# Kernel optimization log

Hardware: AMD Instinct MI355X
Metric: run time of the kernel (lower is better)

Reference implementation:

```python
import jax, jax.numpy as jnp
import numpy as np

# Mamba block hyperparams (canonical: expand=2, d_state=16, d_conv=4, dt_rank=d_model/16)
D_MODEL = 1024
D_INNER = 2 * D_MODEL          # 2048
D_STATE = 16
D_CONV = 4
DT_RANK = D_MODEL // 16        # 64
B, L = 2, 1024


def setup_inputs() -> dict:
    key = jax.random.key(0)
    ks = jax.random.split(key, 12)
    s = lambda fan_in: 1.0 / np.sqrt(fan_in)
    x = jax.random.normal(ks[0], (B, L, D_MODEL), dtype=jnp.float32)
    W_in = jax.random.normal(ks[1], (D_MODEL, 2 * D_INNER), dtype=jnp.float32) * s(D_MODEL)
    conv_w = jax.random.normal(ks[2], (D_INNER, 1, D_CONV), dtype=jnp.float32) * s(D_CONV)
    conv_b = jax.random.normal(ks[3], (D_INNER,), dtype=jnp.float32) * 0.02
    W_xp = jax.random.normal(ks[4], (D_INNER, DT_RANK + 2 * D_STATE), dtype=jnp.float32) * s(D_INNER)
    W_dt = jax.random.normal(ks[5], (DT_RANK, D_INNER), dtype=jnp.float32) * s(DT_RANK)
    # dt bias init so softplus(dt_bias) ~ uniform in [1e-3, 1e-1] (mamba convention)
    dt = jnp.exp(jax.random.uniform(ks[6], (D_INNER,)) * (np.log(0.1) - np.log(1e-3)) + np.log(1e-3))
    dt_bias = dt + jnp.log(-jnp.expm1(-dt))  # inverse softplus
    A_log = jnp.log(jnp.broadcast_to(jnp.arange(1, D_STATE + 1, dtype=jnp.float32), (D_INNER, D_STATE)))
    D_skip = jnp.ones((D_INNER,), dtype=jnp.float32)
    W_out = jax.random.normal(ks[7], (D_INNER, D_MODEL), dtype=jnp.float32) * s(D_INNER)
    return {"x": x, "W_in": W_in, "conv_w": conv_w, "conv_b": conv_b, "W_xp": W_xp,
            "W_dt": W_dt, "dt_bias": dt_bias, "A_log": A_log, "D_skip": D_skip, "W_out": W_out}


def _causal_depthwise_conv(u, conv_w, conv_b):
    # u: [B, E, L], conv_w: [E, 1, K] depthwise, causal (left-pad K-1)
    K = conv_w.shape[-1]
    u = jnp.pad(u, ((0, 0), (0, 0), (K - 1, 0)))
    y = jax.lax.conv_general_dilated(
        u, conv_w, window_strides=(1,), padding='VALID',
        dimension_numbers=('NCH', 'OIH', 'NCH'), feature_group_count=u.shape[1])
    return y + conv_b[None, :, None]


def _selective_scan(u, delta, A, Bm, Cm, D_skip):
    # u, delta: [B,L,E]; A: [E,N]; Bm, Cm: [B,L,N]; D_skip: [E]
    dA = jnp.exp(jnp.einsum('ble,en->blen', delta, A))          # [B,L,E,N]
    dBu = jnp.einsum('ble,bln,ble->blen', delta, Bm, u)          # [B,L,E,N]

    def step(h, inp):
        dA_t, dBu_t, C_t = inp                                    # [B,E,N],[B,E,N],[B,N]
        h = dA_t * h + dBu_t
        y_t = jnp.einsum('ben,bn->be', h, C_t)
        return h, y_t

    h0 = jnp.zeros((u.shape[0], A.shape[0], A.shape[1]), dtype=u.dtype)
    xs = (jnp.swapaxes(dA, 0, 1), jnp.swapaxes(dBu, 0, 1), jnp.swapaxes(Cm, 0, 1))
    _, ys = jax.lax.scan(step, h0, xs)                            # ys: [L,B,E]
    y = jnp.swapaxes(ys, 0, 1)                                    # [B,L,E]
    return y + u * D_skip[None, None, :]


def reference(x, W_in, conv_w, conv_b, W_xp, W_dt, dt_bias, A_log, D_skip, W_out):
    # in_proj and gate split
    xz = x @ W_in                                                 # [B,L,2E]
    xp, z = jnp.split(xz, 2, axis=-1)                             # [B,L,E] each
    # causal depthwise conv + silu
    u = _causal_depthwise_conv(jnp.swapaxes(xp, 1, 2), conv_w, conv_b)
    u = jax.nn.silu(jnp.swapaxes(u, 1, 2))                        # [B,L,E]
    # input-dependent dt, B, C
    x_dbl = u @ W_xp                                              # [B,L,R+2N]
    dt_r, Bm, Cm = jnp.split(x_dbl, [DT_RANK, DT_RANK + D_STATE], axis=-1)
    delta = jax.nn.softplus(dt_r @ W_dt + dt_bias)                # [B,L,E]
    A = -jnp.exp(A_log)                                           # [E,N]
    y = _selective_scan(u, delta, A, Bm, Cm, D_skip)              # [B,L,E]
    # gate and out_proj
    y = y * jax.nn.silu(z)
    return y @ W_out                                              # [B,L,D]
```

## Files before the change

### kernel.cpp

```cpp
#include <hip/hip_runtime.h>
#include <math.h>

#define D_MODEL 1024
#define D_INNER 2048
#define D_STATE 16
#define D_CONV  4
#define DT_RANK 64
#define BB      2
#define LL      1024
#define BL      (BB*LL)
#define CHUNK   16
#define NCHUNK  (LL/CHUNK)
#define KSPLIT  16

typedef __attribute__((ext_vector_type(8))) short short8;
typedef __attribute__((ext_vector_type(4))) float f32x4;
typedef unsigned short ushort_t;
typedef unsigned int uint_t;

__device__ __forceinline__ float sigmoidf_(float x) { return 1.0f / (1.0f + __expf(-x)); }

__device__ __forceinline__ ushort_t f2bf(float f) {
    uint_t u = __float_as_uint(f);
    uint_t r = (u + 0x7fffu + ((u >> 16) & 1u)) >> 16;
    return (ushort_t)r;
}

__device__ __forceinline__ void gload_lds16(const void* g, void* l) {
    __builtin_amdgcn_global_load_lds(
        (const __attribute__((address_space(1))) void*)g,
        (__attribute__((address_space(3))) void*)l,
        16, 0, 0);
}

template<int BM, int BN, int SPLIT>
__global__ __launch_bounds__(256)
void gemm_bf16_t(const ushort_t* __restrict__ A, const ushort_t* __restrict__ Bt,
                 float* __restrict__ C0, float* __restrict__ C1,
                 int M, int N, int K, int split) {
    constexpr int WMr = BM / 32;
    constexpr int WNr = BN / 32;
    const int nx = N / BN;
    const int nwg = nx * (M / BM);
    const int wg = ((blockIdx.x & 7) * (nwg >> 3)) + (blockIdx.x >> 3);
    const int row0 = (wg / nx) * BM;
    const int col0 = (wg % nx) * BN;

    __shared__ __align__(16) ushort_t As[BM * 32];
    __shared__ __align__(16) ushort_t Bs[BN * 32];

    const int tid  = threadIdx.x;
    const int lane = tid & 63;
    const int wave = tid >> 6;
    const int wr = wave >> 1, wc = wave & 1;

    f32x4 acc[WMr][WNr];
    #pragma unroll
    for (int m = 0; m < WMr; ++m)
        #pragma unroll
        for (int n = 0; n < WNr; ++n)
            acc[m][n] = (f32x4){0.f, 0.f, 0.f, 0.f};

    const ushort_t* Ablk = A  + (size_t)row0 * K;
    const ushort_t* Bblk = Bt + (size_t)col0 * K;
    const int r_ld  = tid >> 2;
    const int c8_ld = (tid & 3) * 8;

    for (int k0 = 0; k0 < K; k0 += 32) {
        #pragma unroll
        for (int i = 0; i < BM / 64; ++i)
            gload_lds16(Ablk + (size_t)(i * 64 + r_ld) * K + k0 + c8_ld,
                        &As[(i * 64 + wave * 16) * 32]);
        #pragma unroll
        for (int i = 0; i < BN / 64; ++i)
            gload_lds16(Bblk + (size_t)(i * 64 + r_ld) * K + k0 + c8_ld,
                        &Bs[(i * 64 + wave * 16) * 32]);
        __syncthreads();

        short8 af[WMr], bf[WNr];
        const int fr = lane & 15;
        const int kb = (lane >> 4) * 8;
        #pragma unroll
        for (int m = 0; m < WMr; ++m)
            af[m] = *(const short8*)&As[(wr * WMr * 16 + m * 16 + fr) * 32 + kb];
        #pragma unroll
        for (int n = 0; n < WNr; ++n)
            bf[n] = *(const short8*)&Bs[(wc * WNr * 16 + n * 16 + fr) * 32 + kb];

        #pragma unroll
        for (int m = 0; m < WMr; ++m)
            #pragma unroll
            for (int n = 0; n < WNr; ++n)
                acc[m][n] = __builtin_amdgcn_mfma_f32_16x16x32_bf16(
                    af[m], bf[n], acc[m][n], 0, 0, 0);
        __syncthreads();
    }

    float* Cb; int ldc, cb;
    if (SPLIT && col0 >= split) { Cb = C1; ldc = N - split; cb = col0 - split; }
    else if (SPLIT)             { Cb = C0; ldc = split;     cb = col0; }
    else                        { Cb = C0; ldc = N;         cb = col0; }

    const int crow = (lane >> 4) * 4;
    const int ccol = lane & 15;
    #pragma unroll
    for (int m = 0; m < WMr; ++m) {
        #pragma unroll
        for (int n = 0; n < WNr; ++n) {
            float* cp = Cb + (size_t)(row0 + wr * WMr * 16 + m * 16 + crow) * ldc
                           + cb + wc * WNr * 16 + n * 16 + ccol;
            #pragma unroll
            for (int i = 0; i < 4; ++i)
                cp[(size_t)i * ldc] = acc[m][n][i];
        }
    }
}

__global__ __launch_bounds__(256)
void f32_to_bf16(const float* __restrict__ in, ushort_t* __restrict__ out, int n) {
    int i = (blockIdx.x * 256 + threadIdx.x) * 8;
    if (i + 8 <= n) {
        float4 a = *reinterpret_cast<const float4*>(in + i);
        float4 b = *reinterpret_cast<const float4*>(in + i + 4);
        ushort_t o[8] = {f2bf(a.x), f2bf(a.y), f2bf(a.z), f2bf(a.w),
                         f2bf(b.x), f2bf(b.y), f2bf(b.z), f2bf(b.w)};
        *reinterpret_cast<short8*>(out + i) = *reinterpret_cast<short8*>(o);
    }
}

__global__ __launch_bounds__(256)
void transp_bf16(const float* __restrict__ W, ushort_t* __restrict__ Wt,
                 int R, int C) {
    __shared__ ushort_t tile[32][33];
    int tx = threadIdx.x & 31, ty = threadIdx.x >> 5;
    int r0 = blockIdx.y * 32, c0 = blockIdx.x * 32;
    #pragma unroll
    for (int i = 0; i < 32; i += 8)
        tile[ty + i][tx] = f2bf(W[(size_t)(r0 + ty + i) * C + c0 + tx]);
    __syncthreads();
    #pragma unroll
    for (int i = 0; i < 32; i += 8)
        Wt[(size_t)(c0 + ty + i) * R + r0 + tx] = tile[tx][ty + i];
}

__global__ __launch_bounds__(256)
void gemm_xdbl_splitk(const float* __restrict__ u, const float* __restrict__ W,
                      float* __restrict__ part) {
    __shared__ float As[16][65];
    __shared__ float Bs[16][96];

    const int tid = threadIdx.x;
    const int m0 = blockIdx.x * 64;
    const int kbase = blockIdx.y * (D_INNER / KSPLIT);

    const int tx = tid & 15;
    const int ty = tid >> 4;
    const int arow = tid >> 4;
    const int acol = tid & 15;

    float acc[4][6] = {};

    for (int k0 = 0; k0 < D_INNER / KSPLIT; k0 += 16) {
        #pragma unroll
        for (int p = 0; p < 4; ++p) {
            int r = arow + p * 16;
            As[acol][r] = u[(size_t)(m0 + r) * D_INNER + kbase + k0 + acol];
        }
        #pragma unroll
        for (int j = 0; j < 6; ++j) {
            int idx = j * 256 + tid;
            int row = idx / 96, col = idx - row * 96;
            Bs[row][col] = W[(size_t)(kbase + k0 + row) * 96 + col];
        }
        __syncthreads();
        #pragma unroll
        for (int kk = 0; kk < 16; ++kk) {
            float a[4], b[6];
            #pragma unroll
            for (int i = 0; i < 4; ++i) a[i] = As[kk][ty * 4 + i];
            #pragma unroll
            for (int j = 0; j < 6; ++j) b[j] = Bs[kk][tx * 6 + j];
            #pragma unroll
            for (int i = 0; i < 4; ++i)
                #pragma unroll
                for (int j = 0; j < 6; ++j)
                    acc[i][j] = fmaf(a[i], b[j], acc[i][j]);
        }
        __syncthreads();
    }

    float* pblk = part + (size_t)blockIdx.y * BL * 96;
    #pragma unroll
    for (int i = 0; i < 4; ++i)
        #pragma unroll
        for (int j = 0; j < 6; ++j)
            pblk[(size_t)(m0 + ty * 4 + i) * 96 + tx * 6 + j] = acc[i][j];
}

__global__ __launch_bounds__(256)
void xdbl_reduce(const float* __restrict__ part, float* __restrict__ x_dbl) {
    int i = blockIdx.x * 256 + threadIdx.x;
    float s = 0.0f;
    #pragma unroll
    for (int k = 0; k < KSPLIT; ++k)
        s += part[(size_t)k * BL * 96 + i];
    x_dbl[i] = s;
}

template<int EPI>
__global__ __launch_bounds__(256)
void gemm_f32(const float* __restrict__ A, const float* __restrict__ B,
              float* __restrict__ C, const float* __restrict__ bias,
              int M, int N, int K, int lda, int ldb, int ldc) {
    __shared__ float As[16][65];
    __shared__ float Bs[16][64];

    const int tid = threadIdx.x;
    const int tx = tid & 15;
    const int ty = tid >> 4;
    const int row0 = blockIdx.y * 64;
    const int col0 = blockIdx.x * 64;

    const int arow = tid >> 4;
    const int acol = tid & 15;
    const int brow = tid >> 6;
    const int bcol = tid & 63;

    float acc[4][4] = {};

    for (int k0 = 0; k0 < K; k0 += 16) {
        #pragma unroll
        for (int p = 0; p < 4; ++p) {
            int r = arow + p * 16;
            As[acol][r] = A[(size_t)(row0 + r) * lda + (k0 + acol)];
        }
        int gc = col0 + bcol;
        #pragma unroll
        for (int p = 0; p < 4; ++p) {
            int r = brow + p * 4;
            Bs[r][bcol] = (gc < N) ? B[(size_t)(k0 + r) * ldb + gc] : 0.0f;
        }
        __syncthreads();
        #pragma unroll
        for (int kk = 0; kk < 16; ++kk) {
            float a[4];
            #pragma unroll
            for (int i = 0; i < 4; ++i) a[i] = As[kk][ty * 4 + i];
            float4 bv = *reinterpret_cast<const float4*>(&Bs[kk][tx * 4]);
            float b4[4] = {bv.x, bv.y, bv.z, bv.w};
            #pragma unroll
            for (int i = 0; i < 4; ++i)
                #pragma unroll
                for (int j = 0; j < 4; ++j)
                    acc[i][j] = fmaf(a[i], b4[j], acc[i][j]);
        }
        __syncthreads();
    }

    #pragma unroll
    for (int i = 0; i < 4; ++i) {
        int gr = row0 + ty * 4 + i;
        #pragma unroll
        for (int j = 0; j < 4; ++j) {
            int gc = col0 + tx * 4 + j;
            if (gc < N) {
                float v = acc[i][j];
                if (EPI == 1) {
                    v += bias[gc];
                    v = (v > 20.0f) ? v : log1pf(__expf(v));
                }
                C[(size_t)gr * ldc + gc] = v;
            }
        }
    }
}

__global__ __launch_bounds__(256)
void conv_silu(const float* __restrict__ xp, const float* __restrict__ conv_w,
               const float* __restrict__ conv_b, float* __restrict__ u) {
    int idx = blockIdx.x * 256 + threadIdx.x;
    if (idx >= BL * D_INNER) return;
    int e  = idx & (D_INNER - 1);
    int bl = idx >> 11;
    int b = bl >> 10, l = bl & (LL - 1);
    float acc = conv_b[e];
    #pragma unroll
    for (int k = 0; k < D_CONV; ++k) {
        int ll = l - (D_CONV - 1) + k;
        if (ll >= 0)
            acc = fmaf(conv_w[e * D_CONV + k],
                       xp[(size_t)(b * LL + ll) * D_INNER + e], acc);
    }
    u[idx] = acc * sigmoidf_(acc);
}

__global__ __launch_bounds__(256)
void scan_phase1(const float* __restrict__ delta, const float* __restrict__ u_in,
                 const float* __restrict__ x_dbl, const float* __restrict__ A_log,
                 float* __restrict__ hend, float* __restrict__ sumdelta) {
    int g = blockIdx.x * 256 + threadIdx.x;
    int e = g & (D_INNER - 1);
    int c = (g >> 11) & (NCHUNK - 1);
    int b = g >> 17;

    float A_en[D_STATE];
    #pragma unroll
    for (int n = 0; n < D_STATE; n += 4) {
        float4 al = *(const float4*)&A_log[e * D_STATE + n];
        A_en[n]     = -__expf(al.x);
        A_en[n + 1] = -__expf(al.y);
        A_en[n + 2] = -__expf(al.z);
        A_en[n + 3] = -__expf(al.w);
    }

    float h[D_STATE];
    #pragma unroll
    for (int n = 0; n < D_STATE; ++n) h[n] = 0.0f;
    float S = 0.0f;

    const int t0 = c * CHUNK;
    const float* dptr = delta + (size_t)(b * LL + t0) * D_INNER + e;
    const float* uptr = u_in  + (size_t)(b * LL + t0) * D_INNER + e;
    const float* xb   = x_dbl + (size_t)(b * LL + t0) * 96 + DT_RANK;

    for (int t = 0; t < CHUNK; ++t) {
        float dv = dptr[(size_t)t * D_INNER];
        float uv = uptr[(size_t)t * D_INNER];
        const float* xrow = xb + (size_t)t * 96;
        float4 B0 = *(const float4*)(xrow);
        float4 B1 = *(const float4*)(xrow + 4);
        float4 B2 = *(const float4*)(xrow + 8);
        float4 B3 = *(const float4*)(xrow + 12);
        float Bv[16] = {B0.x, B0.y, B0.z, B0.w, B1.x, B1.y, B1.z, B1.w,
                        B2.x, B2.y, B2.z, B2.w, B3.x, B3.y, B3.z, B3.w};
        S += dv;
        float du = dv * uv;
        #pragma unroll
        for (int n = 0; n < D_STATE; ++n) {
            float dA = __expf(dv * A_en[n]);
            h[n] = fmaf(dA, h[n], du * Bv[n]);
        }
    }

    size_t rbase = ((size_t)(c * BB + b) * D_STATE) * D_INNER + e;
    #pragma unroll
    for (int n = 0; n < D_STATE; ++n)
        hend[rbase + (size_t)n * D_INNER] = h[n];
    sumdelta[(size_t)(c * BB + b) * D_INNER + e] = S;
}

__global__ __launch_bounds__(256)
void scan_phase2(const float* __restrict__ A_log, const float* __restrict__ sumdelta,
                 float* __restrict__ hh) {
    int g = blockIdx.x * 256 + threadIdx.x;
    int e = g & (D_INNER - 1);
    int n = (g >> 11) & (D_STATE - 1);
    int b = g >> 15;
    float A_en = -__expf(A_log[e * D_STATE + n]);
    float h = 0.0f;
    for (int c = 0; c < NCHUNK; ++c) {
        size_t idx = ((size_t)(c * BB + b) * D_STATE + n) * D_INNER + e;
        float he = hh[idx];
        float dA = __expf(A_en * sumdelta[(size_t)(c * BB + b) * D_INNER + e]);
        hh[idx] = h;
        h = fmaf(dA, h, he);
    }
}

__global__ __launch_bounds__(256)
void scan_phase3(const float* __restrict__ delta, const float* __restrict__ u_in,
                 const float* __restrict__ x_dbl, const float* __restrict__ z,
                 const float* __restrict__ A_log, const float* __restrict__ D_skip,
                 const float* __restrict__ hin, ushort_t* __restrict__ ybf) {
    int g = blockIdx.x * 256 + threadIdx.x;
    int e = g & (D_INNER - 1);
    int c = (g >> 11) & (NCHUNK - 1);
    int b = g >> 17;

    float A_en[D_STATE];
    #pragma unroll
    for (int n = 0; n < D_STATE; n += 4) {
        float4 al = *(const float4*)&A_log[e * D_STATE + n];
        A_en[n]     = -__expf(al.x);
        A_en[n + 1] = -__expf(al.y);
        A_en[n + 2] = -__expf(al.z);
        A_en[n + 3] = -__expf(al.w);
    }
    float D_e = D_skip[e];

    float h[D_STATE];
    size_t rbase = ((size_t)(c * BB + b) * D_STATE) * D_INNER + e;
    #pragma unroll
    for (int n = 0; n < D_STATE; ++n)
        h[n] = hin[rbase + (size_t)n * D_INNER];

    const int t0 = c * CHUNK;
    const float* dptr = delta + (size_t)(b * LL + t0) * D_INNER + e;
    const float* uptr = u_in  + (size_t)(b * LL + t0) * D_INNER + e;
    const float* xb   = x_dbl + (size_t)(b * LL + t0) * 96 + DT_RANK;
    const float* zptr = z     + (size_t)(b * LL + t0) * D_INNER + e;
    ushort_t* yout = ybf + (size_t)(b * LL + t0) * D_INNER + e;

    for (int t = 0; t < CHUNK; ++t) {
        float dv = dptr[(size_t)t * D_INNER];
        float uv = uptr[(size_t)t * D_INNER];
        const float* xrow = xb + (size_t)t * 96;
        float4 B0 = *(const float4*)(xrow);
        float4 B1 = *(const float4*)(xrow + 4);
        float4 B2 = *(const float4*)(xrow + 8);
        float4 B3 = *(const float4*)(xrow + 12);
        float4 C0 = *(const float4*)(xrow + 16);
        float4 C1 = *(const float4*)(xrow + 20);
        float4 C2 = *(const float4*)(xrow + 24);
        float4 C3 = *(const float4*)(xrow + 28);
        float Bv[16] = {B0.x, B0.y, B0.z, B0.w, B1.x, B1.y, B1.z, B1.w,
                        B2.x, B2.y, B2.z, B2.w, B3.x, B3.y, B3.z, B3.w};
        float Cv[16] = {C0.x, C0.y, C0.z, C0.w, C1.x, C1.y, C1.z, C1.w,
                        C2.x, C2.y, C2.z, C2.w, C3.x, C3.y, C3.z, C3.w};
        float du = dv * uv;
        float y = 0.0f;
        #pragma unroll
        for (int n = 0; n < D_STATE; ++n) {
            float dA = __expf(dv * A_en[n]);
            h[n] = fmaf(dA, h[n], du * Bv[n]);
            y = fmaf(h[n], Cv[n], y);
        }
        float zv = zptr[(size_t)t * D_INNER];
        float yg = (y + uv * D_e) * (zv * sigmoidf_(zv));
        yout[(size_t)t * D_INNER] = f2bf(yg);
    }
}

extern "C" void kernel_launch(void* const* d_in, const int* in_sizes, int n_in,
                              void* d_out, int out_size, void* d_ws, size_t ws_size,
                              hipStream_t stream) {
    const float* x      = (const float*)d_in[0];
    const float* W_in   = (const float*)d_in[1];
    const float* conv_w = (const float*)d_in[2];
    const float* conv_b = (const float*)d_in[3];
    const float* W_xp   = (const float*)d_in[4];
    const float* W_dt   = (const float*)d_in[5];
    const float* dt_b   = (const float*)d_in[6];
    const float* A_log  = (const float*)d_in[7];
    const float* D_skip = (const float*)d_in[8];
    const float* W_out  = (const float*)d_in[9];
    float* out = (float*)d_out;

    const size_t M1 = 1024 * 1024;
    float* ws    = (float*)d_ws;
    float* z     = ws;
    float* hend  = ws + 4 * M1;
    float* xp    = hend;
    float* u     = ws + 8 * M1;
    float* x_dbl = ws + 12 * M1;
    float* sumd  = x_dbl + (size_t)BL * 96;
    ushort_t* ybf = (ushort_t*)(sumd + BB * NCHUNK * D_INNER);
    float* delta = ws + (14 * M1 + 512 * 1024);

    ushort_t* Wint_bf   = (ushort_t*)delta;
    ushort_t* x_bf      = (ushort_t*)(delta + 2 * M1);
    float*    xdbl_part = delta;
    ushort_t* Woutt_bf  = (ushort_t*)hend;

    dim3 blk(256);

    hipLaunchKernelGGL(f32_to_bf16, dim3((BL * D_MODEL) / (256 * 8)), blk, 0, stream,
                       x, x_bf, BL * D_MODEL);
    hipLaunchKernelGGL(transp_bf16, dim3(4096 / 32, 1024 / 32), blk, 0, stream,
                       W_in, Wint_bf, 1024, 4096);
    hipLaunchKernelGGL((gemm_bf16_t<64, 128, 1>),
                       dim3((BL / 64) * (4096 / 128)), blk, 0, stream,
                       x_bf, Wint_bf, xp, z, BL, 2 * D_INNER, D_MODEL, D_INNER);
    hipLaunchKernelGGL(conv_silu, dim3((BL * D_INNER) / 256), blk, 0, stream,
                       xp, conv_w, conv_b, u);
    hipLaunchKernelGGL(gemm_xdbl_splitk, dim3(BL / 64, KSPLIT), blk, 0, stream,
                       u, W_xp, xdbl_part);
    hipLaunchKernelGGL(xdbl_reduce, dim3((BL * 96) / 256), blk, 0, stream,
                       xdbl_part, x_dbl);
    hipLaunchKernelGGL((gemm_f32<1>), dim3(D_INNER / 64, BL / 64), blk, 0, stream,
                       x_dbl, W_dt, delta, dt_b, BL, D_INNER, DT_RANK, 96, D_INNER, D_INNER);
    hipLaunchKernelGGL(scan_phase1, dim3((BB * NCHUNK * D_INNER) / 256), blk, 0, stream,
                       delta, u, x_dbl, A_log, hend, sumd);
    hipLaunchKernelGGL(scan_phase2, dim3((BB * D_STATE * D_INNER) / 256), blk, 0, stream,
                       A_log, sumd, hend);
    hipLaunchKernelGGL(scan_phase3, dim3((BB * NCHUNK * D_INNER) / 256), blk, 0, stream,
                       delta, u, x_dbl, z, A_log, D_skip, hend, ybf);
    hipLaunchKernelGGL(transp_bf16, dim3(1024 / 32, 2048 / 32), blk, 0, stream,
                       W_out, Woutt_bf, 2048, 1024);
    hipLaunchKernelGGL((gemm_bf16_t<64, 64, 0>),
                       dim3((BL / 64) * (D_MODEL / 64)), blk, 0, stream,
                       ybf, Woutt_bf, out, out, BL, D_MODEL, D_INNER, D_MODEL);
}
```

Before: 197.0 us.

## Fuse conv+SiLU into consumers, store z in bf16, use geometric decay when A=-(n+1)

Removes the standalone conv_silu kernel and its u buffer. The conv and SiLU are now recomputed inside the x_dbl GEMM, with a 3-row halo staged in LDS, and inside both scan phases via a sliding window over xp. The in-projection GEMM writes the gate z as bf16, which halves that buffer's traffic but loses precision in the gate. The scan phases test at runtime whether A equals -(n+1) and, if so, replace 16 exps per step with one exp and repeated multiplies, which relies on the canonical A_log init.

Result: faster. 185.1 us (-6.0%).

```diff
diff --git a/kernel.cpp b/kernel.cpp
--- a/kernel.cpp
+++ b/kernel.cpp
@@ -12,6 +12,7 @@
 #define CHUNK   16
 #define NCHUNK  (LL/CHUNK)
 #define KSPLIT  16
+#define KS_E    (D_INNER/KSPLIT)
 
 typedef __attribute__((ext_vector_type(8))) short short8;
 typedef __attribute__((ext_vector_type(4))) float f32x4;
@@ -24,6 +25,9 @@
     uint_t u = __float_as_uint(f);
     uint_t r = (u + 0x7fffu + ((u >> 16) & 1u)) >> 16;
     return (ushort_t)r;
+}
+__device__ __forceinline__ float bf2f(ushort_t v) {
+    return __uint_as_float((uint_t)v << 16);
 }
 
 __device__ __forceinline__ void gload_lds16(const void* g, void* l) {
@@ -33,10 +37,10 @@
         16, 0, 0);
 }
 
-template<int BM, int BN, int SPLIT>
+template<int BM, int BN, int SPLIT, int BF0, int BF1>
 __global__ __launch_bounds__(256)
 void gemm_bf16_t(const ushort_t* __restrict__ A, const ushort_t* __restrict__ Bt,
-                 float* __restrict__ C0, float* __restrict__ C1,
+                 void* __restrict__ C0v, void* __restrict__ C1v,
                  int M, int N, int K, int split) {
     constexpr int WMr = BM / 32;
     constexpr int WNr = BN / 32;
@@ -96,22 +100,35 @@
         __syncthreads();
     }
 
-    float* Cb; int ldc, cb;
-    if (SPLIT && col0 >= split) { Cb = C1; ldc = N - split; cb = col0 - split; }
-    else if (SPLIT)             { Cb = C0; ldc = split;     cb = col0; }
-    else                        { Cb = C0; ldc = N;         cb = col0; }
-
     const int crow = (lane >> 4) * 4;
     const int ccol = lane & 15;
+    const bool second = SPLIT && (col0 >= split);
+    const int ldc = second ? (N - split) : (SPLIT ? split : N);
+    const int cb  = second ? (col0 - split) : col0;
+
     #pragma unroll
     for (int m = 0; m < WMr; ++m) {
         #pragma unroll
         for (int n = 0; n < WNr; ++n) {
-            float* cp = Cb + (size_t)(row0 + wr * WMr * 16 + m * 16 + crow) * ldc
-                           + cb + wc * WNr * 16 + n * 16 + ccol;
-            #pragma unroll
-            for (int i = 0; i < 4; ++i)
-                cp[(size_t)i * ldc] = acc[m][n][i];
+            size_t base = (size_t)(row0 + wr * WMr * 16 + m * 16 + crow) * ldc
+                          + cb + wc * WNr * 16 + n * 16 + ccol;
+            if (second) {
+                if (BF1) { ushort_t* cp = (ushort_t*)C1v + base;
+                    #pragma unroll
+                    for (int i = 0; i < 4; ++i) cp[(size_t)i * ldc] = f2bf(acc[m][n][i]);
+                } else { float* cp = (float*)C1v + base;
+                    #pragma unroll
+                    for (int i = 0; i < 4; ++i) cp[(size_t)i * ldc] = acc[m][n][i];
+                }
+            } else {
+                if (BF0) { ushort_t* cp = (ushort_t*)C0v + base;
+                    #pragma unroll
+                    for (int i = 0; i < 4; ++i) cp[(size_t)i * ldc] = f2bf(acc[m][n][i]);
+                } else { float* cp = (float*)C0v + base;
+                    #pragma unroll
+                    for (int i = 0; i < 4; ++i) cp[(size_t)i * ldc] = acc[m][n][i];
+                }
+            }
         }
     }
 }
@@ -144,27 +161,29 @@
 }
 
 __global__ __launch_bounds__(256)
-void gemm_xdbl_splitk(const float* __restrict__ u, const float* __restrict__ W,
-                      float* __restrict__ part) {
-    __shared__ float As[16][65];
+void gemm_xdbl_convfused(const float* __restrict__ xp, const float* __restrict__ W,
+                         const float* __restrict__ conv_w, const float* __restrict__ conv_b,
+                         float* __restrict__ part) {
+    __shared__ float Ax[16][68];
+    __shared__ float Au[16][65];
     __shared__ float Bs[16][96];
 
     const int tid = threadIdx.x;
     const int m0 = blockIdx.x * 64;
-    const int kbase = blockIdx.y * (D_INNER / KSPLIT);
-
+    const int kbase = blockIdx.y * KS_E;
     const int tx = tid & 15;
     const int ty = tid >> 4;
-    const int arow = tid >> 4;
-    const int acol = tid & 15;
+    const bool bhead = (m0 & (LL - 1)) == 0;
 
     float acc[4][6] = {};
 
-    for (int k0 = 0; k0 < D_INNER / KSPLIT; k0 += 16) {
-        #pragma unroll
-        for (int p = 0; p < 4; ++p) {
-            int r = arow + p * 16;
-            As[acol][r] = u[(size_t)(m0 + r) * D_INNER + kbase + k0 + acol];
+    for (int k0 = 0; k0 < KS_E; k0 += 16) {
+        for (int i = tid; i < 67 * 16; i += 256) {
+            int r = i >> 4, k = i & 15;
+            float v = 0.f;
+            if (!(bhead && r < 3))
+                v = xp[(size_t)(m0 - 3 + r) * D_INNER + kbase + k0 + k];
+            Ax[k][r] = v;
         }
         #pragma unroll
         for (int j = 0; j < 6; ++j) {
@@ -173,11 +192,26 @@
             Bs[row][col] = W[(size_t)(kbase + k0 + row) * 96 + col];
         }
         __syncthreads();
+        {
+            float4 w4 = *(const float4*)&conv_w[(size_t)(kbase + k0 + tx) * 4];
+            float cbv = conv_b[kbase + k0 + tx];
+            #pragma unroll
+            for (int rr = 0; rr < 4; ++rr) {
+                int r = ty + rr * 16;
+                float a = cbv;
+                a = fmaf(w4.x, Ax[tx][r], a);
+                a = fmaf(w4.y, Ax[tx][r + 1], a);
+                a = fmaf(w4.z, Ax[tx][r + 2], a);
+                a = fmaf(w4.w, Ax[tx][r + 3], a);
+                Au[tx][r] = a * sigmoidf_(a);
+            }
+        }
+        __syncthreads();
         #pragma unroll
         for (int kk = 0; kk < 16; ++kk) {
             float a[4], b[6];
             #pragma unroll
-            for (int i = 0; i < 4; ++i) a[i] = As[kk][ty * 4 + i];
+            for (int i = 0; i < 4; ++i) a[i] = Au[kk][ty * 4 + i];
             #pragma unroll
             for (int j = 0; j < 6; ++j) b[j] = Bs[kk][tx * 6 + j];
             #pragma unroll
@@ -276,26 +310,8 @@
 }
 
 __global__ __launch_bounds__(256)
-void conv_silu(const float* __restrict__ xp, const float* __restrict__ conv_w,
-               const float* __restrict__ conv_b, float* __restrict__ u) {
-    int idx = blockIdx.x * 256 + threadIdx.x;
-    if (idx >= BL * D_INNER) return;
-    int e  = idx & (D_INNER - 1);
-    int bl = idx >> 11;
-    int b = bl >> 10, l = bl & (LL - 1);
-    float acc = conv_b[e];
-    #pragma unroll
-    for (int k = 0; k < D_CONV; ++k) {
-        int ll = l - (D_CONV - 1) + k;
-        if (ll >= 0)
-            acc = fmaf(conv_w[e * D_CONV + k],
-                       xp[(size_t)(b * LL + ll) * D_INNER + e], acc);
-    }
-    u[idx] = acc * sigmoidf_(acc);
-}
-
-__global__ __launch_bounds__(256)
-void scan_phase1(const float* __restrict__ delta, const float* __restrict__ u_in,
+void scan_phase1(const float* __restrict__ delta, const float* __restrict__ xp,
+                 const float* __restrict__ conv_w, const float* __restrict__ conv_b,
                  const float* __restrict__ x_dbl, const float* __restrict__ A_log,
                  float* __restrict__ hend, float* __restrict__ sumdelta) {
     int g = blockIdx.x * 256 + threadIdx.x;
@@ -304,6 +320,7 @@
     int b = g >> 17;
 
     float A_en[D_STATE];
+    bool geo = true;
     #pragma unroll
     for (int n = 0; n < D_STATE; n += 4) {
         float4 al = *(const float4*)&A_log[e * D_STATE + n];
@@ -312,33 +329,78 @@
         A_en[n + 2] = -__expf(al.z);
         A_en[n + 3] = -__expf(al.w);
     }
+    #pragma unroll
+    for (int n = 0; n < D_STATE; ++n)
+        geo = geo && (fabsf(A_en[n] + (float)(n + 1)) <= 2e-5f * (float)(n + 1));
+
+    const int t0 = c * CHUNK;
+    const float* dptr = delta + (size_t)(b * LL + t0) * D_INNER + e;
+    const float* xptr = xp    + (size_t)(b * LL + t0) * D_INNER + e;
+    const float* xb   = x_dbl + (size_t)(b * LL + t0) * 96 + DT_RANK;
+    float4 w4 = *(const float4*)&conv_w[(size_t)e * 4];
+    float cbv = conv_b[e];
+
+    float xw0 = 0.f, xw1 = 0.f, xw2 = 0.f;
+    if (c > 0) {
+        xw0 = xptr[-3 * D_INNER];
+        xw1 = xptr[-2 * D_INNER];
+        xw2 = xptr[-1 * D_INNER];
+    }
 
     float h[D_STATE];
     #pragma unroll
     for (int n = 0; n < D_STATE; ++n) h[n] = 0.0f;
     float S = 0.0f;
 
-    const int t0 = c * CHUNK;
-    const float* dptr = delta + (size_t)(b * LL + t0) * D_INNER + e;
-    const float* uptr = u_in  + (size_t)(b * LL + t0) * D_INNER + e;
-    const float* xb   = x_dbl + (size_t)(b * LL + t0) * 96 + DT_RANK;
-
-    for (int t = 0; t < CHUNK; ++t) {
-        float dv = dptr[(size_t)t * D_INNER];
-        float uv = uptr[(size_t)t * D_INNER];
-        const float* xrow = xb + (size_t)t * 96;
-        float4 B0 = *(const float4*)(xrow);
-        float4 B1 = *(const float4*)(xrow + 4);
-        float4 B2 = *(const float4*)(xrow + 8);
-        float4 B3 = *(const float4*)(xrow + 12);
-        float Bv[16] = {B0.x, B0.y, B0.z, B0.w, B1.x, B1.y, B1.z, B1.w,
-                        B2.x, B2.y, B2.z, B2.w, B3.x, B3.y, B3.z, B3.w};
-        S += dv;
-        float du = dv * uv;
-        #pragma unroll
-        for (int n = 0; n < D_STATE; ++n) {
-            float dA = __expf(dv * A_en[n]);
-            h[n] = fmaf(dA, h[n], du * Bv[n]);
+    if (geo) {
+        for (int t = 0; t < CHUNK; ++t) {
+            float dv = dptr[(size_t)t * D_INNER];
+            float x0 = xptr[(size_t)t * D_INNER];
+            float a = cbv;
+            a = fmaf(w4.x, xw0, a); a = fmaf(w4.y, xw1, a);
+            a = fmaf(w4.z, xw2, a); a = fmaf(w4.w, x0, a);
+            float uv = a * sigmoidf_(a);
+            xw0 = xw1; xw1 = xw2; xw2 = x0;
+            const float* xrow = xb + (size_t)t * 96;
+            float4 B0 = *(const float4*)(xrow);
+            float4 B1 = *(const float4*)(xrow + 4);
+            float4 B2 = *(const float4*)(xrow + 8);
+            float4 B3 = *(const float4*)(xrow + 12);
+            float Bv[16] = {B0.x, B0.y, B0.z, B0.w, B1.x, B1.y, B1.z, B1.w,
+                            B2.x, B2.y, B2.z, B2.w, B3.x, B3.y, B3.z, B3.w};
+            S += dv;
+            float du = dv * uv;
+            float q = __expf(-dv);
+            float dA = q;
+            #pragma unroll
+            for (int n = 0; n < D_STATE; ++n) {
+                h[n] = fmaf(dA, h[n], du * Bv[n]);
+                dA *= q;
+            }
+        }
+    } else {
+        for (int t = 0; t < CHUNK; ++t) {
+            float dv = dptr[(size_t)t * D_INNER];
+            float x0 = xptr[(size_t)t * D_INNER];
+            float a = cbv;
+            a = fmaf(w4.x, xw0, a); a = fmaf(w4.y, xw1, a);
+            a = fmaf(w4.z, xw2, a); a = fmaf(w4.w, x0, a);
+            float uv = a * sigmoidf_(a);
+            xw0 = xw1; xw1 = xw2; xw2 = x0;
+            const float* xrow = xb + (size_t)t * 96;
+            float4 B0 = *(const float4*)(xrow);
+            float4 B1 = *(const float4*)(xrow + 4);
+            float4 B2 = *(const float4*)(xrow + 8);
+            float4 B3 = *(const float4*)(xrow + 12);
+            float Bv[16] = {B0.x, B0.y, B0.z, B0.w, B1.x, B1.y, B1.z, B1.w,
+                            B2.x, B2.y, B2.z, B2.w, B3.x, B3.y, B3.z, B3.w};
+            S += dv;
+            float du = dv * uv;
+            #pragma unroll
+            for (int n = 0; n < D_STATE; ++n) {
+                float dA = __expf(dv * A_en[n]);
+                h[n] = fmaf(dA, h[n], du * Bv[n]);
+            }
         }
     }
 
@@ -357,6 +419,8 @@
     int n = (g >> 11) & (D_STATE - 1);
     int b = g >> 15;
     float A_en = -__expf(A_log[e * D_STATE + n]);
+    float np1 = (float)(n + 1);
+    if (fabsf(A_en + np1) <= 2e-5f * np1) A_en = -np1;
     float h = 0.0f;
     for (int c = 0; c < NCHUNK; ++c) {
         size_t idx = ((size_t)(c * BB + b) * D_STATE + n) * D_INNER + e;
@@ -368,8 +432,9 @@
 }
 
 __global__ __launch_bounds__(256)
-void scan_phase3(const float* __restrict__ delta, const float* __restrict__ u_in,
-                 const float* __restrict__ x_dbl, const float* __restrict__ z,
+void scan_phase3(const float* __restrict__ delta, const float* __restrict__ xp,
+                 const float* __restrict__ conv_w, const float* __restrict__ conv_b,
+                 const float* __restrict__ x_dbl, const ushort_t* __restrict__ zbf,
                  const float* __restrict__ A_log, const float* __restrict__ D_skip,
                  const float* __restrict__ hin, ushort_t* __restrict__ ybf) {
     int g = blockIdx.x * 256 + threadIdx.x;
@@ -378,6 +443,7 @@
     int b = g >> 17;
 
     float A_en[D_STATE];
+    bool geo = true;
     #pragma unroll
     for (int n = 0; n < D_STATE; n += 4) {
         float4 al = *(const float4*)&A_log[e * D_STATE + n];
@@ -386,8 +452,11 @@
         A_en[n + 2] = -__expf(al.z);
         A_en[n + 3] = -__expf(al.w);
     }
+    #pragma unroll
+    for (int n = 0; n < D_STATE; ++n)
+        geo = geo && (fabsf(A_en[n] + (float)(n + 1)) <= 2e-5f * (float)(n + 1));
+
     float D_e = D_skip[e];
-
     float h[D_STATE];
     size_t rbase = ((size_t)(c * BB + b) * D_STATE) * D_INNER + e;
     #pragma unroll
@@ -396,38 +465,90 @@
 
     const int t0 = c * CHUNK;
     const float* dptr = delta + (size_t)(b * LL + t0) * D_INNER + e;
-    const float* uptr = u_in  + (size_t)(b * LL + t0) * D_INNER + e;
+    const float* xptr = xp    + (size_t)(b * LL + t0) * D_INNER + e;
     const float* xb   = x_dbl + (size_t)(b * LL + t0) * 96 + DT_RANK;
-    const float* zptr = z     + (size_t)(b * LL + t0) * D_INNER + e;
+    const ushort_t* zptr = zbf + (size_t)(b * LL + t0) * D_INNER + e;
     ushort_t* yout = ybf + (size_t)(b * LL + t0) * D_INNER + e;
-
-    for (int t = 0; t < CHUNK; ++t) {
-        float dv = dptr[(size_t)t * D_INNER];
-        float uv = uptr[(size_t)t * D_INNER];
-        const float* xrow = xb + (size_t)t * 96;
-        float4 B0 = *(const float4*)(xrow);
-        float4 B1 = *(const float4*)(xrow + 4);
-        float4 B2 = *(const float4*)(xrow + 8);
-        float4 B3 = *(const float4*)(xrow + 12);
-        float4 C0 = *(const float4*)(xrow + 16);
-        float4 C1 = *(const float4*)(xrow + 20);
-        float4 C2 = *(const float4*)(xrow + 24);
-        float4 C3 = *(const float4*)(xrow + 28);
-        float Bv[16] = {B0.x, B0.y, B0.z, B0.w, B1.x, B1.y, B1.z, B1.w,
-                        B2.x, B2.y, B2.z, B2.w, B3.x, B3.y, B3.z, B3.w};
-        float Cv[16] = {C0.x, C0.y, C0.z, C0.w, C1.x, C1.y, C1.z, C1.w,
-                        C2.x, C2.y, C2.z, C2.w, C3.x, C3.y, C3.z, C3.w};
-        float du = dv * uv;
-        float y = 0.0f;
-        #pragma unroll
-        for (int n = 0; n < D_STATE; ++n) {
-            float dA = __expf(dv * A_en[n]);
-            h[n] = fmaf(dA, h[n], du * Bv[n]);
-            y = fmaf(h[n], Cv[n], y);
-        }
-        float zv = zptr[(size_t)t * D_INNER];
-        float yg = (y + uv * D_e) * (zv * sigmoidf_(zv));
-        yout[(size_t)t * D_INNER] = f2bf(yg);
+    float4 w4 = *(const float4*)&conv_w[(size_t)e * 4];
+    float cbv = conv_b[e];
+
+    float xw0 = 0.f, xw1 = 0.f, xw2 = 0.f;
+    if (c > 0) {
+        xw0 = xptr[-3 * D_INNER];
+        xw1 = xptr[-2 * D_INNER];
+        xw2 = xptr[-1 * D_INNER];
+    }
+
+    if (geo) {
+        for (int t = 0; t < CHUNK; ++t) {
+            float dv = dptr[(size_t)t * D_INNER];
+            float x0 = xptr[(size_t)t * D_INNER];
+            float a = cbv;
+            a = fmaf(w4.x, xw0, a); a = fmaf(w4.y, xw1, a);
+            a = fmaf(w4.z, xw2, a); a = fmaf(w4.w, x0, a);
+            float uv = a * sigmoidf_(a);
+            xw0 = xw1; xw1 = xw2; xw2 = x0;
+            const float* xrow = xb + (size_t)t * 96;
+            float4 B0 = *(const float4*)(xrow);
+            float4 B1 = *(const float4*)(xrow + 4);
+            float4 B2 = *(const float4*)(xrow + 8);
+            float4 B3 = *(const float4*)(xrow + 12);
+            float4 C0 = *(const float4*)(xrow + 16);
+            float4 C1 = *(const float4*)(xrow + 20);
+            float4 C2 = *(const float4*)(xrow + 24);
+            float4 C3 = *(const float4*)(xrow + 28);
+            float Bv[16] = {B0.x, B0.y, B0.z, B0.w, B1.x, B1.y, B1.z, B1.w,
+                            B2.x, B2.y, B2.z, B2.w, B3.x, B3.y, B3.z, B3.w};
+            float Cv[16] = {C0.x, C0.y, C0.z, C0.w, C1.x, C1.y, C1.z, C1.w,
+                            C2.x, C2.y, C2.z, C2.w, C3.x, C3.y, C3.z, C3.w};
+            float du = dv * uv;
+            float q = __expf(-dv);
+            float dA = q;
+            float y = 0.0f;
+            #pragma unroll
+            for (int n = 0; n < D_STATE; ++n) {
+                h[n] = fmaf(dA, h[n], du * Bv[n]);
+                y = fmaf(h[n], Cv[n], y);
+                dA *= q;
+            }
+            float zv = bf2f(zptr[(size_t)t * D_INNER]);
+            float yg = (y + uv * D_e) * (zv * sigmoidf_(zv));
+            yout[(size_t)t * D_INNER] = f2bf(yg);
+        }
+    } else {
+        for (int t = 0; t < CHUNK; ++t) {
+            float dv = dptr[(size_t)t * D_INNER];
+            float x0 = xptr[(size_t)t * D_INNER];
+            float a = cbv;
+            a = fmaf(w4.x, xw0, a); a = fmaf(w4.y, xw1, a);
+            a = fmaf(w4.z, xw2, a); a = fmaf(w4.w, x0, a);
+            float uv = a * sigmoidf_(a);
+            xw0 = xw1; xw1 = xw2; xw2 = x0;
+            const float* xrow = xb + (size_t)t * 96;
+            float4 B0 = *(const float4*)(xrow);
+            float4 B1 = *(const float4*)(xrow + 4);
+            float4 B2 = *(const float4*)(xrow + 8);
+            float4 B3 = *(const float4*)(xrow + 12);
+            float4 C0 = *(const float4*)(xrow + 16);
+            float4 C1 = *(const float4*)(xrow + 20);
+            float4 C2 = *(const float4*)(xrow + 24);
+            float4 C3 = *(const float4*)(xrow + 28);
+            float Bv[16] = {B0.x, B0.y, B0.z, B0.w, B1.x, B1.y, B1.z, B1.w,
+                            B2.x, B2.y, B2.z, B2.w, B3.x, B3.y, B3.z, B3.w};
+            float Cv[16] = {C0.x, C0.y, C0.z, C0.w, C1.x, C1.y, C1.z, C1.w,
+                            C2.x, C2.y, C2.z, C2.w, C3.x, C3.y, C3.z, C3.w};
+            float du = dv * uv;
+            float y = 0.0f;
+            #pragma unroll
+            for (int n = 0; n < D_STATE; ++n) {
+                float dA = __expf(dv * A_en[n]);
+                h[n] = fmaf(dA, h[n], du * Bv[n]);
+                y = fmaf(h[n], Cv[n], y);
+            }
+            float zv = bf2f(zptr[(size_t)t * D_INNER]);
+            float yg = (y + uv * D_e) * (zv * sigmoidf_(zv));
+            yout[(size_t)t * D_INNER] = f2bf(yg);
+        }
     }
 }
 
@@ -447,20 +568,18 @@
     float* out = (float*)d_out;
 
     const size_t M1 = 1024 * 1024;
-    float* ws    = (float*)d_ws;
-    float* z     = ws;
-    float* hend  = ws + 4 * M1;
-    float* xp    = hend;
-    float* u     = ws + 8 * M1;
-    float* x_dbl = ws + 12 * M1;
-    float* sumd  = x_dbl + (size_t)BL * 96;
-    ushort_t* ybf = (ushort_t*)(sumd + BB * NCHUNK * D_INNER);
-    float* delta = ws + (14 * M1 + 512 * 1024);
-
-    ushort_t* Wint_bf   = (ushort_t*)delta;
-    ushort_t* x_bf      = (ushort_t*)(delta + 2 * M1);
+    float* ws = (float*)d_ws;
+    float*    xp    = ws;
+    float*    hend  = ws + 4 * M1;
+    float*    delta = ws + 8 * M1;
+    ushort_t* z_bf  = (ushort_t*)(ws + 12 * M1);
+    float*    x_dbl = ws + 14 * M1;
+    float*    sumd  = ws + 14 * M1 + 262144;
+    ushort_t* ybf   = (ushort_t*)(ws + 14 * M1 + 524288);
     float*    xdbl_part = delta;
+    ushort_t* Wint_bf   = (ushort_t*)hend;
     ushort_t* Woutt_bf  = (ushort_t*)hend;
+    ushort_t* x_bf      = ybf;
 
     dim3 blk(256);
 
@@ -468,26 +587,26 @@
                        x, x_bf, BL * D_MODEL);
     hipLaunchKernelGGL(transp_bf16, dim3(4096 / 32, 1024 / 32), blk, 0, stream,
                        W_in, Wint_bf, 1024, 4096);
-    hipLaunchKernelGGL((gemm_bf16_t<64, 128, 1>),
+    hipLaunchKernelGGL((gemm_bf16_t<64, 128, 1, 0, 1>),
                        dim3((BL / 64) * (4096 / 128)), blk, 0, stream,
-                       x_bf, Wint_bf, xp, z, BL, 2 * D_INNER, D_MODEL, D_INNER);
-    hipLaunchKernelGGL(conv_silu, dim3((BL * D_INNER) / 256), blk, 0, stream,
-                       xp, conv_w, conv_b, u);
-    hipLaunchKernelGGL(gemm_xdbl_splitk, dim3(BL / 64, KSPLIT), blk, 0, stream,
-                       u, W_xp, xdbl_part);
+                       x_bf, Wint_bf, (void*)xp, (void*)z_bf,
+                       BL, 2 * D_INNER, D_MODEL, D_INNER);
+    hipLaunchKernelGGL(gemm_xdbl_convfused, dim3(BL / 64, KSPLIT), blk, 0, stream,
+                       xp, W_xp, conv_w, conv_b, xdbl_part);
     hipLaunchKernelGGL(xdbl_reduce, dim3((BL * 96) / 256), blk, 0, stream,
                        xdbl_part, x_dbl);
     hipLaunchKernelGGL((gemm_f32<1>), dim3(D_INNER / 64, BL / 64), blk, 0, stream,
                        x_dbl, W_dt, delta, dt_b, BL, D_INNER, DT_RANK, 96, D_INNER, D_INNER);
     hipLaunchKernelGGL(scan_phase1, dim3((BB * NCHUNK * D_INNER) / 256), blk, 0, stream,
-                       delta, u, x_dbl, A_log, hend, sumd);
+                       delta, xp, conv_w, conv_b, x_dbl, A_log, hend, sumd);
     hipLaunchKernelGGL(scan_phase2, dim3((BB * D_STATE * D_INNER) / 256), blk, 0, stream,
                        A_log, sumd, hend);
     hipLaunchKernelGGL(scan_phase3, dim3((BB * NCHUNK * D_INNER) / 256), blk, 0, stream,
-                       delta, u, x_dbl, z, A_log, D_skip, hend, ybf);
+                       delta, xp, conv_w, conv_b, x_dbl, z_bf, A_log, D_skip, hend, ybf);
     hipLaunchKernelGGL(transp_bf16, dim3(1024 / 32, 2048 / 32), blk, 0, stream,
                        W_out, Woutt_bf, 2048, 1024);
-    hipLaunchKernelGGL((gemm_bf16_t<64, 64, 0>),
+    hipLaunchKernelGGL((gemm_bf16_t<64, 64, 0, 0, 0>),
                        dim3((BL / 64) * (D_MODEL / 64)), blk, 0, stream,
-                       ybf, Woutt_bf, out, out, BL, D_MODEL, D_INNER, D_MODEL);
-}
+                       ybf, Woutt_bf, (void*)out, (void*)out,
+                       BL, D_MODEL, D_INNER, D_MODEL);
+}
```
